# Optimization experiments

Hardware: AMD Instinct MI355X
Metric: run time of the kernel (lower is better)

The kernel has to match this reference:

```python
import jax, jax.numpy as jnp
import numpy as np

ALPHA = 3.0
NITERS = 15
POWER_ITERS = 20
ROOTS = [np.cos(np.pi * (2 * i + 1) / (2 * NITERS)) for i in range(NITERS)]


def batch_conv2d(inputs, kernels):
    # inputs: [B,1,H,W], kernels: [B,1,3,3]; per-sample 3x3 stencil via grouped conv
    B, _, H, W = inputs.shape
    out = jax.lax.conv_general_dilated(
        inputs.reshape(1, B, H, W), kernels,
        window_strides=(1, 1), padding=((1, 1), (1, 1)),
        feature_group_count=B,
        dimension_numbers=("NCHW", "OIHW", "NCHW"))
    return out.reshape(B, 1, H, W)


def setup_inputs() -> dict:
    key = jax.random.key(0)
    k1, k2, k3, k4 = jax.random.split(key, 4)
    B, H, W = 64, 512, 512
    x = jax.random.normal(k1, (B, 1, H, W), dtype=jnp.float32)
    f = jax.random.normal(k2, (B, 1, H, W), dtype=jnp.float32)
    kernelA = jax.random.normal(k3, (B, 1, 3, 3), dtype=jnp.float32)
    u = jax.random.normal(k4, (B, 1, H, W), dtype=jnp.float32)
    return {"x": x, "f": f, "kernelA": kernelA, "u": u}


def reference(x, f, kernelA, u):
    # Power iteration to estimate the dominant eigenvalue magnitude m per sample
    for _ in range(POWER_ITERS):
        y = batch_conv2d(u, kernelA)
        m = jnp.max(jnp.abs(y), axis=(2, 3), keepdims=True)  # [B,1,1,1]
        u = y / m
    # Chebyshev step sizes over the band [m/alpha, m]
    taus = jnp.stack(
        [2.0 / (m + m / ALPHA - (m / ALPHA - m) * r) for r in ROOTS])  # [niters,B,1,1,1]

    def cheby_step(xc, tau):
        Ax = batch_conv2d(xc, kernelA)
        return xc + tau * (f - Ax), None

    x, _ = jax.lax.scan(cheby_step, x, taus)
    return x
```

## Files before the change

### kernel.cpp

```cpp
#include <hip/hip_runtime.h>

#define BB 64
#define HH 512
#define WW 512
#define PLANE (HH * WW)
#define N_CHEBY 15
#define FD 5
#define RR 32
#define NS (HH / RR)
#define STEPS (RR + 2 * FD)

struct F8 { float v[8]; };

__device__ __forceinline__ float wshr1(float x) {
    return __int_as_float(__builtin_amdgcn_update_dpp(
        0, __float_as_int(x), 0x138, 0xF, 0xF, true));
}
__device__ __forceinline__ float wshl1(float x) {
    return __int_as_float(__builtin_amdgcn_update_dpp(
        0, __float_as_int(x), 0x130, 0xF, 0xF, true));
}

__device__ __forceinline__ F8 ldrow(const float* plane, int y, int lane, bool ok) {
    F8 r;
    if (ok) {
        const float4* p =
            reinterpret_cast<const float4*>(plane + (size_t)y * WW + (lane << 3));
        const float4 a = p[0], b = p[1];
        r.v[0] = a.x; r.v[1] = a.y; r.v[2] = a.z; r.v[3] = a.w;
        r.v[4] = b.x; r.v[5] = b.y; r.v[6] = b.z; r.v[7] = b.w;
    } else {
#pragma unroll
        for (int i = 0; i < 8; ++i) r.v[i] = 0.f;
    }
    return r;
}

__device__ __forceinline__ void racc8(const F8& r, float k0, float k1, float k2,
                                      float acc[8]) {
    const float lf = wshr1(r.v[7]);
    const float rt = wshl1(r.v[0]);
    acc[0] = fmaf(k0, lf, fmaf(k1, r.v[0], fmaf(k2, r.v[1], acc[0])));
#pragma unroll
    for (int c = 1; c < 7; ++c)
        acc[c] = fmaf(k0, r.v[c-1], fmaf(k1, r.v[c], fmaf(k2, r.v[c+1], acc[c])));
    acc[7] = fmaf(k0, r.v[6], fmaf(k1, r.v[7], fmaf(k2, rt, acc[7])));
}

__global__ __launch_bounds__(256, 1) void conv_wave(
    const float* __restrict__ in, const float* __restrict__ kern,
    const float* __restrict__ pm_prev, float* __restrict__ out,
    float* __restrict__ pmw, float* __restrict__ pmz)
{
    const int lane = threadIdx.x & 63;
    const int wid  = threadIdx.x >> 6;
    const int b = blockIdx.y;
    const int stripe = (blockIdx.x << 2) + wid;
    const int ytop = stripe * RR;

    float invv = 1.f;
    if (pm_prev) {
        float v = (lane < NS) ? pm_prev[b * NS + lane] : 0.f;
#pragma unroll
        for (int o = 32; o; o >>= 1) v = fmaxf(v, __shfl_xor(v, o, 64));
        invv = 1.f / v;
    }

    const float* kb = kern + b * 9;
    const float k00=kb[0],k01=kb[1],k02=kb[2],k10=kb[3],k11=kb[4],k12=kb[5],
                k20=kb[6],k21=kb[7],k22=kb[8];
    const float* ip = in + (size_t)b * PLANE;
    float* op = out ? out + (size_t)b * PLANE : nullptr;

    F8 u2 = {}, u1 = {};
    F8 lt[FD - 1] = {}, lm[FD - 1] = {};
    float mz = 0.f, mw = 0.f;
    F8 u0 = ldrow(ip, ytop - FD, lane, (unsigned)(ytop - FD) < HH);

#pragma unroll 6
    for (int p = 0; p < STEPS; ++p) {
        const int yL = ytop - FD + p;
        F8 un = ldrow(ip, yL + 1, lane,
                      (p < STEPS - 1) && ((unsigned)(yL + 1) < HH));

        F8 nw[FD - 1];
        {
            float acc[8] = {0,0,0,0,0,0,0,0};
            racc8(u2, k00,k01,k02, acc);
            racc8(u1, k10,k11,k12, acc);
            racc8(u0, k20,k21,k22, acc);
            const int y = yL - 1;
            const bool act = (y >= ytop - (FD-1)) && (y <= ytop + RR + FD - 2)
                          && ((unsigned)y < HH);
#pragma unroll
            for (int c = 0; c < 8; ++c) nw[0].v[c] = act ? acc[c] * invv : 0.f;
        }
#pragma unroll
        for (int j = 2; j <= FD; ++j) {
            float acc[8] = {0,0,0,0,0,0,0,0};
            racc8(lt[j-2], k00,k01,k02, acc);
            racc8(lm[j-2], k10,k11,k12, acc);
            racc8(nw[j-2], k20,k21,k22, acc);
            const int y = yL - j;
            if (j < FD) {
                const bool act = (y >= ytop - (FD-j)) && (y <= ytop + RR + FD - j - 1)
                              && ((unsigned)y < HH);
#pragma unroll
                for (int c = 0; c < 8; ++c) nw[j-1].v[c] = act ? acc[c] : 0.f;
                if (j == FD - 1) {
#pragma unroll
                    for (int c = 0; c < 8; ++c)
                        mz = fmaxf(mz, fabsf(nw[j-1].v[c]));
                }
            } else {
                if (y >= ytop && y < ytop + RR) {
#pragma unroll
                    for (int c = 0; c < 8; ++c) mw = fmaxf(mw, fabsf(acc[c]));
                    if (op) {
                        float4* q = reinterpret_cast<float4*>(
                            op + (size_t)y * WW + (lane << 3));
                        q[0] = make_float4(acc[0], acc[1], acc[2], acc[3]);
                        q[1] = make_float4(acc[4], acc[5], acc[6], acc[7]);
                    }
                }
            }
        }
#pragma unroll
        for (int l = 0; l < FD - 1; ++l) { lt[l] = lm[l]; lm[l] = nw[l]; }
        u2 = u1; u1 = u0; u0 = un;
    }

#pragma unroll
    for (int o = 32; o; o >>= 1) {
        mz = fmaxf(mz, __shfl_xor(mz, o, 64));
        mw = fmaxf(mw, __shfl_xor(mw, o, 64));
    }
    if (lane == 0) {
        pmz[b * NS + stripe] = mz;
        pmw[b * NS + stripe] = mw;
    }
}

__global__ __launch_bounds__(64) void tau_k(
    const float* __restrict__ pmz, const float* __restrict__ pmw,
    float* __restrict__ taus)
{
    const int b = blockIdx.x, t = threadIdx.x;
    float vz = (t < NS) ? pmz[b * NS + t] : 0.f;
    float vw = (t < NS) ? pmw[b * NS + t] : 0.f;
#pragma unroll
    for (int o = 32; o; o >>= 1) {
        vz = fmaxf(vz, __shfl_xor(vz, o, 64));
        vw = fmaxf(vw, __shfl_xor(vw, o, 64));
    }
    if (t < N_CHEBY) {
        const float m = vw / vz;
        const double rr = cos(M_PI * (2.0 * t + 1.0) / (2.0 * N_CHEBY));
        const float denom = m + m / 3.0f - (m / 3.0f - m) * (float)rr;
        taus[t * BB + b] = 2.0f / denom;
    }
}

__global__ __launch_bounds__(256, 1) void cheby_wave(
    const float* __restrict__ xin, const float* __restrict__ fin,
    const float* __restrict__ kern, const float* __restrict__ tauv,
    float* __restrict__ xout)
{
    __shared__ float fring[4][FD + 1][WW];
    const int lane = threadIdx.x & 63;
    const int wid  = threadIdx.x >> 6;
    const int b = blockIdx.y;
    const int stripe = (blockIdx.x << 2) + wid;
    const int ytop = stripe * RR;
    float* fr = &fring[wid][0][0];

    const float* kb = kern + b * 9;
    const float k00=kb[0],k01=kb[1],k02=kb[2],k10=kb[3],k11=kb[4],k12=kb[5],
                k20=kb[6],k21=kb[7],k22=kb[8];
    float tau[FD];
#pragma unroll
    for (int j = 0; j < FD; ++j) tau[j] = tauv[j * BB + b];

    const float* xp = xin + (size_t)b * PLANE;
    const float* fp = fin + (size_t)b * PLANE;
    float* op = xout + (size_t)b * PLANE;

    F8 u2 = {}, u1 = {};
    F8 lt[FD - 1] = {}, lm[FD - 1] = {};
    F8 u0 = ldrow(xp, ytop - FD, lane, (unsigned)(ytop - FD) < HH);

#pragma unroll 6
    for (int p = 0; p < STEPS; ++p) {
        const int yL = ytop - FD + p;
        F8 un = ldrow(xp, yL + 1, lane,
                      (p < STEPS - 1) && ((unsigned)(yL + 1) < HH));
        F8 fn = ldrow(fp, yL, lane, (p < STEPS - 1) && ((unsigned)yL < HH));

        F8 ft[FD];
#pragma unroll
        for (int j = 1; j <= FD; ++j) {
            const int sp = (p + (FD + 1) - j) % (FD + 1);
            const float4* q =
                reinterpret_cast<const float4*>(&fr[sp * WW + (lane << 3)]);
            const float4 a = q[0], bb = q[1];
            ft[j-1].v[0] = a.x; ft[j-1].v[1] = a.y;
            ft[j-1].v[2] = a.z; ft[j-1].v[3] = a.w;
            ft[j-1].v[4] = bb.x; ft[j-1].v[5] = bb.y;
            ft[j-1].v[6] = bb.z; ft[j-1].v[7] = bb.w;
        }

        F8 nw[FD - 1];
        {
            float acc[8] = {0,0,0,0,0,0,0,0};
            racc8(u2, k00,k01,k02, acc);
            racc8(u1, k10,k11,k12, acc);
            racc8(u0, k20,k21,k22, acc);
            const int y = yL - 1;
            const bool act = (y >= ytop - (FD-1)) && (y <= ytop + RR + FD - 2)
                          && ((unsigned)y < HH);
#pragma unroll
            for (int c = 0; c < 8; ++c)
                nw[0].v[c] = act ? fmaf(tau[0], ft[0].v[c] - acc[c], u1.v[c]) : 0.f;
        }
#pragma unroll
        for (int j = 2; j <= FD; ++j) {
            float acc[8] = {0,0,0,0,0,0,0,0};
            racc8(lt[j-2], k00,k01,k02, acc);
            racc8(lm[j-2], k10,k11,k12, acc);
            racc8(nw[j-2], k20,k21,k22, acc);
            const int y = yL - j;
            if (j < FD) {
                const bool act = (y >= ytop - (FD-j)) && (y <= ytop + RR + FD - j - 1)
                              && ((unsigned)y < HH);
#pragma unroll
                for (int c = 0; c < 8; ++c)
                    nw[j-1].v[c] =
                        act ? fmaf(tau[j-1], ft[j-1].v[c] - acc[c], lm[j-2].v[c])
                            : 0.f;
            } else {
                if (y >= ytop && y < ytop + RR) {
                    float4* q = reinterpret_cast<float4*>(
                        op + (size_t)y * WW + (lane << 3));
                    float o0 = fmaf(tau[FD-1], ft[FD-1].v[0] - acc[0], lm[j-2].v[0]);
                    float o1 = fmaf(tau[FD-1], ft[FD-1].v[1] - acc[1], lm[j-2].v[1]);
                    float o2 = fmaf(tau[FD-1], ft[FD-1].v[2] - acc[2], lm[j-2].v[2]);
                    float o3 = fmaf(tau[FD-1], ft[FD-1].v[3] - acc[3], lm[j-2].v[3]);
                    q[0] = make_float4(o0, o1, o2, o3);
                    o0 = fmaf(tau[FD-1], ft[FD-1].v[4] - acc[4], lm[j-2].v[4]);
                    o1 = fmaf(tau[FD-1], ft[FD-1].v[5] - acc[5], lm[j-2].v[5]);
                    o2 = fmaf(tau[FD-1], ft[FD-1].v[6] - acc[6], lm[j-2].v[6]);
                    o3 = fmaf(tau[FD-1], ft[FD-1].v[7] - acc[7], lm[j-2].v[7]);
                    q[1] = make_float4(o0, o1, o2, o3);
                }
            }
        }

        if (p < STEPS - 1) {
            float4* q = reinterpret_cast<float4*>(
                &fr[(p % (FD + 1)) * WW + (lane << 3)]);
            q[0] = make_float4(fn.v[0], fn.v[1], fn.v[2], fn.v[3]);
            q[1] = make_float4(fn.v[4], fn.v[5], fn.v[6], fn.v[7]);
        }

#pragma unroll
        for (int l = 0; l < FD - 1; ++l) { lt[l] = lm[l]; lm[l] = nw[l]; }
        u2 = u1; u1 = u0; u0 = un;
    }
}

extern "C" void kernel_launch(void* const* d_in, const int* in_sizes, int n_in,
                              void* d_out, int out_size, void* d_ws, size_t ws_size,
                              hipStream_t stream)
{
    const float* x_in = (const float*)d_in[0];
    const float* f_in = (const float*)d_in[1];
    const float* k_in = (const float*)d_in[2];
    const float* u_in = (const float*)d_in[3];
    float* out = (float*)d_out;

    float* bufA = (float*)d_ws;
    float* pmW0 = bufA + (size_t)BB * PLANE;
    float* pmW1 = pmW0 + BB * NS;
    float* pmZ  = pmW1 + BB * NS;
    float* taus = pmZ  + BB * NS;

    dim3 blk(256), grd(NS / 4, BB);

    conv_wave<<<grd, blk, 0, stream>>>(u_in, k_in, nullptr, bufA, pmW0, pmZ);
    conv_wave<<<grd, blk, 0, stream>>>(bufA, k_in, pmW0, out,  pmW1, pmZ);
    conv_wave<<<grd, blk, 0, stream>>>(out,  k_in, pmW1, bufA, pmW0, pmZ);
    conv_wave<<<grd, blk, 0, stream>>>(bufA, k_in, pmW0, nullptr, pmW1, pmZ);

    tau_k<<<BB, 64, 0, stream>>>(pmZ, pmW1, taus);

    cheby_wave<<<grd, blk, 0, stream>>>(x_in, f_in, k_in, taus,          out);
    cheby_wave<<<grd, blk, 0, stream>>>(out,  f_in, k_in, taus + 5 * BB, bufA);
    cheby_wave<<<grd, blk, 0, stream>>>(bufA, f_in, k_in, taus + 10 * BB, out);
}
```

Baseline: 383.7 us.

## Halve Chebyshev stripe height, transpose LDS ring layout, allow two blocks per CU

The Chebyshev wavefront kernel becomes a template on stripe height and is launched with 16-row stripes instead of 32, so the grid has twice as many blocks. Launch bounds now allow two blocks per CU and the unroll factor drops from 6 to 2, which should free registers and raise occupancy. The f ring buffer in LDS is laid out channel-major ([8][64]), so each lane does strided scalar accesses instead of float4 loads, which should avoid bank conflicts. In exchange, the 2*FD halo rows are recomputed over fewer output rows, adding redundant conv work and extra global reads.

Result: faster. 343.2 us (-10.5%).

```diff
diff --git a/kernel.cpp b/kernel.cpp
--- a/kernel.cpp
+++ b/kernel.cpp
@@ -161,18 +161,21 @@
     }
 }
 
-__global__ __launch_bounds__(256, 1) void cheby_wave(
+template<int RRv>
+__global__ __launch_bounds__(256, 2) void cheby_wave2(
     const float* __restrict__ xin, const float* __restrict__ fin,
     const float* __restrict__ kern, const float* __restrict__ tauv,
     float* __restrict__ xout)
 {
-    __shared__ float fring[4][FD + 1][WW];
+    constexpr int NSv = HH / RRv;
+    constexpr int STEPSv = RRv + 2 * FD;
+    __shared__ float fring[4][FD + 1][8][64];
     const int lane = threadIdx.x & 63;
     const int wid  = threadIdx.x >> 6;
     const int b = blockIdx.y;
     const int stripe = (blockIdx.x << 2) + wid;
-    const int ytop = stripe * RR;
-    float* fr = &fring[wid][0][0];
+    const int ytop = stripe * RRv;
+    float (*fr)[8][64] = fring[wid];
 
     const float* kb = kern + b * 9;
     const float k00=kb[0],k01=kb[1],k02=kb[2],k10=kb[3],k11=kb[4],k12=kb[5],
@@ -189,24 +192,19 @@
     F8 lt[FD - 1] = {}, lm[FD - 1] = {};
     F8 u0 = ldrow(xp, ytop - FD, lane, (unsigned)(ytop - FD) < HH);
 
-#pragma unroll 6
-    for (int p = 0; p < STEPS; ++p) {
+#pragma unroll 2
+    for (int p = 0; p < STEPSv; ++p) {
         const int yL = ytop - FD + p;
         F8 un = ldrow(xp, yL + 1, lane,
-                      (p < STEPS - 1) && ((unsigned)(yL + 1) < HH));
-        F8 fn = ldrow(fp, yL, lane, (p < STEPS - 1) && ((unsigned)yL < HH));
+                      (p < STEPSv - 1) && ((unsigned)(yL + 1) < HH));
+        F8 fn = ldrow(fp, yL, lane, (p < STEPSv - 1) && ((unsigned)yL < HH));
 
         F8 ft[FD];
 #pragma unroll
         for (int j = 1; j <= FD; ++j) {
             const int sp = (p + (FD + 1) - j) % (FD + 1);
-            const float4* q =
-                reinterpret_cast<const float4*>(&fr[sp * WW + (lane << 3)]);
-            const float4 a = q[0], bb = q[1];
-            ft[j-1].v[0] = a.x; ft[j-1].v[1] = a.y;
-            ft[j-1].v[2] = a.z; ft[j-1].v[3] = a.w;
-            ft[j-1].v[4] = bb.x; ft[j-1].v[5] = bb.y;
-            ft[j-1].v[6] = bb.z; ft[j-1].v[7] = bb.w;
+#pragma unroll
+            for (int c = 0; c < 8; ++c) ft[j-1].v[c] = fr[sp][c][lane];
         }
 
         F8 nw[FD - 1];
@@ -216,7 +214,7 @@
             racc8(u1, k10,k11,k12, acc);
             racc8(u0, k20,k21,k22, acc);
             const int y = yL - 1;
-            const bool act = (y >= ytop - (FD-1)) && (y <= ytop + RR + FD - 2)
+            const bool act = (y >= ytop - (FD-1)) && (y <= ytop + RRv + FD - 2)
                           && ((unsigned)y < HH);
 #pragma unroll
             for (int c = 0; c < 8; ++c)
@@ -230,7 +228,7 @@
             racc8(nw[j-2], k20,k21,k22, acc);
             const int y = yL - j;
             if (j < FD) {
-                const bool act = (y >= ytop - (FD-j)) && (y <= ytop + RR + FD - j - 1)
+                const bool act = (y >= ytop - (FD-j)) && (y <= ytop + RRv + FD - j - 1)
                               && ((unsigned)y < HH);
 #pragma unroll
                 for (int c = 0; c < 8; ++c)
@@ -238,7 +236,7 @@
                         act ? fmaf(tau[j-1], ft[j-1].v[c] - acc[c], lm[j-2].v[c])
                             : 0.f;
             } else {
-                if (y >= ytop && y < ytop + RR) {
+                if (y >= ytop && y < ytop + RRv) {
                     float4* q = reinterpret_cast<float4*>(
                         op + (size_t)y * WW + (lane << 3));
                     float o0 = fmaf(tau[FD-1], ft[FD-1].v[0] - acc[0], lm[j-2].v[0]);
@@ -255,11 +253,10 @@
             }
         }
 
-        if (p < STEPS - 1) {
-            float4* q = reinterpret_cast<float4*>(
-                &fr[(p % (FD + 1)) * WW + (lane << 3)]);
-            q[0] = make_float4(fn.v[0], fn.v[1], fn.v[2], fn.v[3]);
-            q[1] = make_float4(fn.v[4], fn.v[5], fn.v[6], fn.v[7]);
+        if (p < STEPSv - 1) {
+            const int sp = p % (FD + 1);
+#pragma unroll
+            for (int c = 0; c < 8; ++c) fr[sp][c][lane] = fn.v[c];
         }
 
 #pragma unroll
@@ -284,16 +281,18 @@
     float* pmZ  = pmW1 + BB * NS;
     float* taus = pmZ  + BB * NS;
 
-    dim3 blk(256), grd(NS / 4, BB);
-
-    conv_wave<<<grd, blk, 0, stream>>>(u_in, k_in, nullptr, bufA, pmW0, pmZ);
-    conv_wave<<<grd, blk, 0, stream>>>(bufA, k_in, pmW0, out,  pmW1, pmZ);
-    conv_wave<<<grd, blk, 0, stream>>>(out,  k_in, pmW1, bufA, pmW0, pmZ);
-    conv_wave<<<grd, blk, 0, stream>>>(bufA, k_in, pmW0, nullptr, pmW1, pmZ);
+    dim3 blk(256);
+    dim3 grdc(NS / 4, BB);
+
+    conv_wave<<<grdc, blk, 0, stream>>>(u_in, k_in, nullptr, bufA, pmW0, pmZ);
+    conv_wave<<<grdc, blk, 0, stream>>>(bufA, k_in, pmW0, out,  pmW1, pmZ);
+    conv_wave<<<grdc, blk, 0, stream>>>(out,  k_in, pmW1, bufA, pmW0, pmZ);
+    conv_wave<<<grdc, blk, 0, stream>>>(bufA, k_in, pmW0, nullptr, pmW1, pmZ);
 
     tau_k<<<BB, 64, 0, stream>>>(pmZ, pmW1, taus);
 
-    cheby_wave<<<grd, blk, 0, stream>>>(x_in, f_in, k_in, taus,          out);
-    cheby_wave<<<grd, blk, 0, stream>>>(out,  f_in, k_in, taus + 5 * BB, bufA);
-    cheby_wave<<<grd, blk, 0, stream>>>(bufA, f_in, k_in, taus + 10 * BB, out);
-}
+    dim3 grdy((HH / 16) / 4, BB);
+    cheby_wave2<16><<<grdy, blk, 0, stream>>>(x_in, f_in, k_in, taus,          out);
+    cheby_wave2<16><<<grdy, blk, 0, stream>>>(out,  f_in, k_in, taus + 5 * BB, bufA);
+    cheby_wave2<16><<<grdy, blk, 0, stream>>>(bufA, f_in, k_in, taus + 10 * BB, out);
+}
```
